# Kernel optimization log

Measured on AMD Instinct MI355X. Metric: run time of the kernel, lower is better.

Reference implementation:

```python
import jax, jax.numpy as jnp
import numpy as np

B, H, W, C = 32, 56, 56, 256
NH, WS, SHIFT = 8, 7, 3
S = WS * WS            # tokens per window = 49
CH = C // NH           # channels per head = 32
EPS = 1e-5


def layer_norm(x, w, b):
    mu = jnp.mean(x, axis=-1, keepdims=True)
    var = jnp.var(x, axis=-1, keepdims=True)
    return (x - mu) * jax.lax.rsqrt(var + EPS) * w + b


def spatial_mlp(x, weight, bias):
    # x: (B, H*W, C); weight: (NH*S, S, 1) grouped-conv1d weight; bias: (NH*S,)
    xr = x.reshape(B, H, W, C)
    if SHIFT > 0:
        P_l, P_r, P_t, P_b = WS - SHIFT, SHIFT, WS - SHIFT, SHIFT
        xr = jnp.pad(xr, ((0, 0), (P_t, P_b), (P_l, P_r), (0, 0)))
    Hp, Wp = xr.shape[1], xr.shape[2]
    # window partition -> (nW, S, NH, CH)
    win = xr.reshape(B, Hp // WS, WS, Wp // WS, WS, C)
    win = win.transpose(0, 1, 3, 2, 4, 5).reshape(-1, S, NH, CH)
    # grouped 1x1 conv == per-head token-mixing matrix (S x S)
    wgt = weight.reshape(NH, S, S)             # wgt[h, i, j]
    out = jnp.einsum('hij,njhd->nihd', wgt, win)
    out = out + bias.reshape(NH, S).T[None, :, :, None]
    # window reverse -> (B, Hp, Wp, C)
    out = out.reshape(B, Hp // WS, Wp // WS, WS, WS, C)
    out = out.transpose(0, 1, 3, 2, 4, 5).reshape(B, Hp, Wp, C)
    if SHIFT > 0:
        out = out[:, P_t:Hp - P_b, P_l:Wp - P_r, :]
    return out.reshape(B, H * W, C)


def mlp(x, fc1_w, fc1_b, fc2_w, fc2_b):
    h = jax.nn.gelu(x @ fc1_w + fc1_b, approximate=False)
    return h @ fc2_w + fc2_b


def setup_inputs() -> dict:
    key = jax.random.key(0)
    ks = jax.random.split(key, 5)
    sc = 0.02
    return {
        'x': jax.random.normal(ks[0], (B, H * W, C), jnp.float32),
        'norm1_w': jnp.ones((C,), jnp.float32),
        'norm1_b': jnp.zeros((C,), jnp.float32),
        'spatial_w': jax.random.normal(ks[1], (NH * S, S, 1), jnp.float32) * sc,
        'spatial_b': jax.random.normal(ks[2], (NH * S,), jnp.float32) * sc,
        'norm2_w': jnp.ones((C,), jnp.float32),
        'norm2_b': jnp.zeros((C,), jnp.float32),
        'fc1_w': jax.random.normal(ks[3], (C, 4 * C), jnp.float32) * sc,
        'fc1_b': jnp.zeros((4 * C,), jnp.float32),
        'fc2_w': jax.random.normal(ks[4], (4 * C, C), jnp.float32) * sc,
        'fc2_b': jnp.zeros((C,), jnp.float32),
    }


def reference(x, norm1_w, norm1_b, spatial_w, spatial_b, norm2_w, norm2_b,
              fc1_w, fc1_b, fc2_w, fc2_b):
    shortcut = x
    h = layer_norm(x, norm1_w, norm1_b)
    h = spatial_mlp(h, spatial_w, spatial_b)
    x = shortcut + h                      # drop_path = 0 (eval)
    x = x + mlp(layer_norm(x, norm2_w, norm2_b), fc1_w, fc1_b, fc2_w, fc2_b)
    return x
```

## Files before the change

### kernel.cpp

```cpp
#include <hip/hip_runtime.h>
#include <hip/hip_bf16.h>

#define NHEAD 8
#define IMG   3136
#define MTOT  100352

typedef __attribute__((ext_vector_type(2))) _Float16 f16x2;
typedef __attribute__((ext_vector_type(8))) _Float16 f16x8;
typedef __attribute__((ext_vector_type(4))) float    f32x4;
typedef __attribute__((ext_vector_type(16))) float   f32x16;
typedef __attribute__((ext_vector_type(8))) short    bf16x8;
typedef __attribute__((ext_vector_type(4))) short    s16x4;
typedef __attribute__((ext_vector_type(4))) int      i32x4;

#define SWZA(byteoff, r) ((byteoff) ^ (((r)&7)<<4) ^ ((((r)>>3)&1)<<7))

__device__ __forceinline__ short f2bf(float f){
  union { float fv; unsigned u; } a; a.fv = f;
  unsigned u = a.u;
  unsigned r = (u + 0x7fffu + ((u >> 16) & 1u)) >> 16;
  return (short)r;
}

__device__ __forceinline__ float dot2f16(f16x2 a, f16x2 b, float c){
#if __has_builtin(__builtin_amdgcn_fdot2)
  return __builtin_amdgcn_fdot2(a, b, c, false);
#else
  return c + (float)a[0]*(float)b[0] + (float)a[1]*(float)b[1];
#endif
}

__device__ __forceinline__ float gelu_f(float v){
  float u = v*(0.7978845608028654f + 0.0356774081f*(v*v));
  float e = __expf(2.f*u);
  float th = 1.f - 2.f/(e + 1.f);
  return 0.5f*v*(1.f + th);
}

__global__ void prep_k(const float* __restrict__ fc1w, const float* __restrict__ fc2w,
                       const float* __restrict__ spw,
                       short* __restrict__ w1p, short* __restrict__ w2p,
                       f16x2* __restrict__ wsp2)
{
  int bid = blockIdx.x, t = threadIdx.x;
  if (bid < 128) {
    int id = bid*256 + t;
    int l = id & 63, fk = id >> 6;
    int kk = fk & 15, f = fk >> 4;
    int n = f*32 + (l & 31);
    int kbase = kk*16 + (l >> 5)*8;
    bf16x8 o;
    #pragma unroll
    for (int e = 0; e < 8; ++e) o[e] = f2bf(fc1w[(size_t)(kbase+e)*1024 + n]);
    *(bf16x8*)(w1p + (size_t)id*8) = o;
  } else if (bid < 256) {
    int id = (bid-128)*256 + t;
    int l = id & 63, fk = id >> 6;
    int kk = fk & 63, f = fk >> 6;
    int n = f*32 + (l & 31);
    int kbase = kk*16 + (l >> 5)*8;
    bf16x8 o;
    #pragma unroll
    for (int e = 0; e < 8; ++e) o[e] = f2bf(fc2w[(size_t)(kbase+e)*256 + n]);
    *(bf16x8*)(w2p + (size_t)id*8) = o;
  } else {
    for (int idx = t; idx < 8*25*52; idx += 256) {
      int h = idx / 1300, rem = idx - h*1300;
      int jpp = rem / 52, i = rem - jpp*52;
      float lo = 0.f, hi = 0.f;
      if (i < 49) {
        int j0 = jpp*2;
        lo = spw[(size_t)(h*49 + i)*49 + j0];
        if (j0 + 1 < 49) hi = spw[(size_t)(h*49 + i)*49 + j0 + 1];
      }
      f16x2 v; v[0] = (_Float16)lo; v[1] = (_Float16)hi;
      wsp2[idx] = v;
    }
  }
}

__global__ __launch_bounds__(512,4) void win_k(
    const float* __restrict__ x, const float* __restrict__ n1w, const float* __restrict__ n1b,
    const float* __restrict__ spb, const f16x2* __restrict__ wsp2,
    float* __restrict__ x1)
{
  extern __shared__ char wsm[];
  char* lx = wsm;
  int t = threadIdx.x, lane = t & 63, wave = t >> 6;
  int bid = blockIdx.x;

  int wi_[2], wj_[2], b_[2];
  #pragma unroll
  for (int w = 0; w < 2; ++w) {
    int win = bid*2 + w;
    b_[w] = win/81; int rem = win - b_[w]*81;
    wi_[w] = rem/9; wj_[w] = rem - (rem/9)*9;
  }

  {
    i32x4 z4 = {0,0,0,0};
    i32x4* lx4 = (i32x4*)lx;
    for (int i = t; i < 3200; i += 512) lx4[i] = z4;
  }
  __syncthreads();

  f32x4 wv = *(const f32x4*)(n1w + lane*4);
  f32x4 bv = *(const f32x4*)(n1b + lane*4);
  #pragma unroll
  for (int w = 0; w < 2; ++w) {
    for (int i = wave; i < 49; i += 8) {
      int iy = i/7, ix = i - iy*7;
      int hh = wi_[w]*7 + iy - 4, ww = wj_[w]*7 + ix - 4;
      if (hh < 0 || hh >= 56 || ww < 0 || ww >= 56) continue;
      const float* row = x + ((size_t)(b_[w]*IMG + hh*56 + ww))*256;
      f32x4 v = *(const f32x4*)(row + lane*4);
      float s  = v[0]+v[1]+v[2]+v[3];
      float s2 = v[0]*v[0]+v[1]*v[1]+v[2]*v[2]+v[3]*v[3];
      #pragma unroll
      for (int m = 1; m < 64; m <<= 1) { s += __shfl_xor(s, m); s2 += __shfl_xor(s2, m); }
      float mu = s * (1.f/256.f);
      float rs = rsqrtf(s2*(1.f/256.f) - mu*mu + 1e-5f);
      char* base = lx + w*25600 + (i>>1)*1024 + (i&1)*2;
      #pragma unroll
      for (int q = 0; q < 4; ++q)
        *(_Float16*)(base + (lane*4+q)*4) = (_Float16)(((v[q]-mu)*rs)*wv[q] + bv[q]);
    }
  }
  __syncthreads();

  int h = __builtin_amdgcn_readfirstlane(wave);
  int d = lane & 31;
  int w = lane >> 5;
  int c = h*32 + d;
  const char* lxW = lx + w*25600 + c*4;
  const char* wgh = (const char*)wsp2 + h*5200;

  float acc[52];
  #pragma unroll
  for (int i = 0; i < 52; ++i) acc[i] = 0.f;

  for (int jpp = 0; jpp < 25; ++jpp) {
    f16x2 xa = *(const f16x2*)(lxW + jpp*1024);
    const char* wrow = wgh + jpp*208;
    #pragma unroll
    for (int ib = 0; ib < 13; ++ib) {
      f16x8 wq = *(const f16x8*)(wrow + ib*16);
      #pragma unroll
      for (int q = 0; q < 4; ++q) {
        f16x2 wp; wp[0] = wq[2*q]; wp[1] = wq[2*q+1];
        acc[ib*4+q] = dot2f16(wp, xa, acc[ib*4+q]);
      }
    }
  }

  int winW = bid*2 + w;
  int bW = winW/81, remW = winW - bW*81, wiW = remW/9, wjW = remW - (remW/9)*9;
  #pragma unroll
  for (int i = 0; i < 49; ++i) {
    int iy = i/7, ix = i - iy*7;
    float sb = spb[h*49 + i];
    int hh = wiW*7 + iy - 4, ww = wjW*7 + ix - 4;
    if (hh >= 0 && hh < 56 && ww >= 0 && ww < 56) {
      size_t off = ((size_t)(bW*IMG + hh*56 + ww))*256 + c;
      x1[off] = x[off] + acc[i] + sb;
    }
  }
}

__global__ __launch_bounds__(512,4) void mlp_k(
    const float* __restrict__ x1, float* __restrict__ out,
    const short* __restrict__ w1p, const short* __restrict__ w2p,
    const float* __restrict__ n2w, const float* __restrict__ n2b,
    const float* __restrict__ b1, const float* __restrict__ b2)
{
  extern __shared__ char sm[];
  char* a2  = sm;
  char* hcb = sm + 32768;

  int t = threadIdx.x, lane = t & 63, wave = t >> 6;
  int m0 = blockIdx.x * 64;

  {
    f32x4 nw = *(const f32x4*)(n2w + lane*4);
    f32x4 nb = *(const f32x4*)(n2b + lane*4);
    #pragma unroll
    for (int rq = 0; rq < 8; ++rq) {
      int rr = wave*8 + rq;
      f32x4 v = *(const f32x4*)(x1 + (size_t)(m0+rr)*256 + lane*4);
      float s  = v[0]+v[1]+v[2]+v[3];
      float s2 = v[0]*v[0]+v[1]*v[1]+v[2]*v[2]+v[3]*v[3];
      #pragma unroll
      for (int m = 1; m < 64; m <<= 1){ s += __shfl_xor(s,m); s2 += __shfl_xor(s2,m); }
      float mu = s*(1.f/256.f);
      float rs = rsqrtf(s2*(1.f/256.f) - mu*mu + 1e-5f);
      s16x4 pk;
      #pragma unroll
      for (int q = 0; q < 4; ++q) pk[q] = f2bf((v[q]-mu)*rs*nw[q] + nb[q]);
      *(s16x4*)(a2 + SWZA(lane*8, rr) + rr*512) = pk;
    }
  }
  __syncthreads();

  int lr = lane & 31, lk = lane >> 5;
  int wn = wave;

  f32x16 accO[2];
  #pragma unroll
  for (int i=0;i<2;++i)
    #pragma unroll
    for (int q=0;q<16;++q) accO[i][q] = 0.f;

  for (int ch = 0; ch < 4; ++ch) {
    f32x16 accH[2];
    #pragma unroll
    for (int i=0;i<2;++i)
      #pragma unroll
      for (int q=0;q<16;++q) accH[i][q] = 0.f;

    const short* w1f = w1p + ((size_t)((ch*8 + wn)*16)*64 + lane)*8;
    bf16x8 bq[4];
    #pragma unroll
    for (int k = 0; k < 4; ++k) bq[k] = *(const bf16x8*)(w1f + (size_t)k*512);
    __builtin_amdgcn_s_setprio(1);
    #pragma unroll
    for (int kk = 0; kk < 16; ++kk) {
      bf16x8 b = bq[kk & 3];
      if (kk < 12) bq[kk & 3] = *(const bf16x8*)(w1f + (size_t)(kk+4)*512);
      int kb = kk*32 + lk*16;
      bf16x8 a0 = *(const bf16x8*)(a2 + SWZA(kb, lr) + lr*512);
      bf16x8 a1 = *(const bf16x8*)(a2 + SWZA(kb, 32+lr) + (32+lr)*512);
      accH[0] = __builtin_amdgcn_mfma_f32_32x32x16_bf16(a0, b, accH[0], 0,0,0);
      accH[1] = __builtin_amdgcn_mfma_f32_32x32x16_bf16(a1, b, accH[1], 0,0,0);
    }
    __builtin_amdgcn_s_setprio(0);

    {
      float b1v = b1[ch*256 + wn*32 + lr];
      int colb = (wn*32 + lr)*2;
      #pragma unroll
      for (int ms = 0; ms < 2; ++ms) {
        #pragma unroll
        for (int r = 0; r < 16; ++r) {
          int rowl = ms*32 + (r&3) + 8*(r>>2) + 4*lk;
          float g = gelu_f(accH[ms][r] + b1v);
          *(short*)(hcb + SWZA(colb, rowl) + rowl*512) = f2bf(g);
        }
      }
    }
    __syncthreads();

    const short* w2f = w2p + ((size_t)(wn*64 + ch*16)*64 + lane)*8;
    #pragma unroll
    for (int k = 0; k < 4; ++k) bq[k] = *(const bf16x8*)(w2f + (size_t)k*512);
    __builtin_amdgcn_s_setprio(1);
    #pragma unroll
    for (int kk = 0; kk < 16; ++kk) {
      bf16x8 b = bq[kk & 3];
      if (kk < 12) bq[kk & 3] = *(const bf16x8*)(w2f + (size_t)(kk+4)*512);
      int kb = kk*32 + lk*16;
      bf16x8 a0 = *(const bf16x8*)(hcb + SWZA(kb, lr) + lr*512);
      bf16x8 a1 = *(const bf16x8*)(hcb + SWZA(kb, 32+lr) + (32+lr)*512);
      accO[0] = __builtin_amdgcn_mfma_f32_32x32x16_bf16(a0, b, accO[0], 0,0,0);
      accO[1] = __builtin_amdgcn_mfma_f32_32x32x16_bf16(a1, b, accO[1], 0,0,0);
    }
    __builtin_amdgcn_s_setprio(0);
    __syncthreads();
  }

  {
    int col = wn*32 + lr;
    float b2v = b2[col];
    #pragma unroll
    for (int ms = 0; ms < 2; ++ms) {
      #pragma unroll
      for (int r = 0; r < 16; ++r) {
        int row = ms*32 + (r&3) + 8*(r>>2) + 4*lk;
        size_t off = (size_t)(m0 + row)*256 + col;
        out[off] = x1[off] + accO[ms][r] + b2v;
      }
    }
  }
}

extern "C" void kernel_launch(void* const* d_in, const int* in_sizes, int n_in,
                              void* d_out, int out_size, void* d_ws, size_t ws_size,
                              hipStream_t stream) {
  const float* x    = (const float*)d_in[0];
  const float* n1w  = (const float*)d_in[1];
  const float* n1b  = (const float*)d_in[2];
  const float* spw  = (const float*)d_in[3];
  const float* spb  = (const float*)d_in[4];
  const float* n2w  = (const float*)d_in[5];
  const float* n2b  = (const float*)d_in[6];
  const float* fc1w = (const float*)d_in[7];
  const float* fc1b = (const float*)d_in[8];
  const float* fc2w = (const float*)d_in[9];
  const float* fc2b = (const float*)d_in[10];
  float* outp = (float*)d_out;

  char* ws = (char*)d_ws;
  short* w1p = (short*)ws;
  short* w2p = (short*)(ws + 524288);
  f16x2* wsp2 = (f16x2*)(ws + 1048576);

  prep_k<<<257, 256, 0, stream>>>(fc1w, fc2w, spw, w1p, w2p, wsp2);

  hipFuncSetAttribute(reinterpret_cast<const void*>(win_k),
                      hipFuncAttributeMaxDynamicSharedMemorySize, 51200);
  win_k<<<1296, 512, 51200, stream>>>(x, n1w, n1b, spb, wsp2, outp);

  hipFuncSetAttribute(reinterpret_cast<const void*>(mlp_k),
                      hipFuncAttributeMaxDynamicSharedMemorySize, 65536);
  mlp_k<<<MTOT/64, 512, 65536, stream>>>(outp, outp, w1p, w2p, n2w, n2b, fc1b, fc2b);
}
```

Baseline: 334.1 us.

## Use bf16 MFMA for window token-mixing instead of fdot2 scalar loops

The per-head 49x49 token-mixing in win_k now runs as bf16 32x32x16 MFMA tiles, padded to 64x64, instead of per-lane fdot2 accumulation over 52 registers. Weights are pre-packed into the MFMA A-operand layout in prep_k. LayerNorm stats are computed first, then normalized activations are written transposed and swizzled into LDS as bf16. This cuts VALU work and register pressure, at the cost of more LDS (66KB per block, which may reduce occupancy), lower precision (bf16 instead of fp16), and uncoalesced per-channel reads of x during the transpose.

```diff
diff --git a/kernel.cpp b/kernel.cpp
--- a/kernel.cpp
+++ b/kernel.cpp
@@ -22,14 +22,6 @@
   return (short)r;
 }
 
-__device__ __forceinline__ float dot2f16(f16x2 a, f16x2 b, float c){
-#if __has_builtin(__builtin_amdgcn_fdot2)
-  return __builtin_amdgcn_fdot2(a, b, c, false);
-#else
-  return c + (float)a[0]*(float)b[0] + (float)a[1]*(float)b[1];
-#endif
-}
-
 __device__ __forceinline__ float gelu_f(float v){
   float u = v*(0.7978845608028654f + 0.0356774081f*(v*v));
   float e = __expf(2.f*u);
@@ -40,7 +32,7 @@
 __global__ void prep_k(const float* __restrict__ fc1w, const float* __restrict__ fc2w,
                        const float* __restrict__ spw,
                        short* __restrict__ w1p, short* __restrict__ w2p,
-                       f16x2* __restrict__ wsp2)
+                       short* __restrict__ wspA)
 {
   int bid = blockIdx.x, t = threadIdx.x;
   if (bid < 128) {
@@ -64,55 +56,47 @@
     for (int e = 0; e < 8; ++e) o[e] = f2bf(fc2w[(size_t)(kbase+e)*256 + n]);
     *(bf16x8*)(w2p + (size_t)id*8) = o;
   } else {
-    for (int idx = t; idx < 8*25*52; idx += 256) {
-      int h = idx / 1300, rem = idx - h*1300;
-      int jpp = rem / 52, i = rem - jpp*52;
-      float lo = 0.f, hi = 0.f;
-      if (i < 49) {
-        int j0 = jpp*2;
-        lo = spw[(size_t)(h*49 + i)*49 + j0];
-        if (j0 + 1 < 49) hi = spw[(size_t)(h*49 + i)*49 + j0 + 1];
-      }
-      f16x2 v; v[0] = (_Float16)lo; v[1] = (_Float16)hi;
-      wsp2[idx] = v;
+    #pragma unroll
+    for (int k = 0; k < 16; ++k) {
+      int idx = t + k*256;
+      int lane = idx & 63;
+      int kt = (idx >> 6) & 3;
+      int mt = (idx >> 8) & 1;
+      int h  = idx >> 9;
+      int i  = mt*32 + (lane & 31);
+      int jb = kt*16 + (lane >> 5)*8;
+      bf16x8 o;
+      #pragma unroll
+      for (int e = 0; e < 8; ++e) {
+        int j = jb + e;
+        float v = (i < 49 && j < 49) ? spw[(size_t)(h*49 + i)*49 + j] : 0.f;
+        o[e] = f2bf(v);
+      }
+      *(bf16x8*)(wspA + (size_t)idx*8) = o;
     }
   }
 }
 
 __global__ __launch_bounds__(512,4) void win_k(
     const float* __restrict__ x, const float* __restrict__ n1w, const float* __restrict__ n1b,
-    const float* __restrict__ spb, const f16x2* __restrict__ wsp2,
+    const float* __restrict__ spb, const short* __restrict__ wspA,
     float* __restrict__ x1)
 {
   extern __shared__ char wsm[];
-  char* lx = wsm;
+  char*  lxT  = wsm;
+  float* murs = (float*)(wsm + 65536);
   int t = threadIdx.x, lane = t & 63, wave = t >> 6;
   int bid = blockIdx.x;
 
-  int wi_[2], wj_[2], b_[2];
   #pragma unroll
   for (int w = 0; w < 2; ++w) {
     int win = bid*2 + w;
-    b_[w] = win/81; int rem = win - b_[w]*81;
-    wi_[w] = rem/9; wj_[w] = rem - (rem/9)*9;
-  }
-
-  {
-    i32x4 z4 = {0,0,0,0};
-    i32x4* lx4 = (i32x4*)lx;
-    for (int i = t; i < 3200; i += 512) lx4[i] = z4;
-  }
-  __syncthreads();
-
-  f32x4 wv = *(const f32x4*)(n1w + lane*4);
-  f32x4 bv = *(const f32x4*)(n1b + lane*4);
-  #pragma unroll
-  for (int w = 0; w < 2; ++w) {
+    int b = win/81, rem = win - b*81, wi = rem/9, wj = rem - (rem/9)*9;
     for (int i = wave; i < 49; i += 8) {
       int iy = i/7, ix = i - iy*7;
-      int hh = wi_[w]*7 + iy - 4, ww = wj_[w]*7 + ix - 4;
+      int hh = wi*7 + iy - 4, ww = wj*7 + ix - 4;
       if (hh < 0 || hh >= 56 || ww < 0 || ww >= 56) continue;
-      const float* row = x + ((size_t)(b_[w]*IMG + hh*56 + ww))*256;
+      const float* row = x + ((size_t)(b*IMG + hh*56 + ww))*256;
       f32x4 v = *(const f32x4*)(row + lane*4);
       float s  = v[0]+v[1]+v[2]+v[3];
       float s2 = v[0]*v[0]+v[1]*v[1]+v[2]*v[2]+v[3]*v[3];
@@ -120,49 +104,80 @@
       for (int m = 1; m < 64; m <<= 1) { s += __shfl_xor(s, m); s2 += __shfl_xor(s2, m); }
       float mu = s * (1.f/256.f);
       float rs = rsqrtf(s2*(1.f/256.f) - mu*mu + 1e-5f);
-      char* base = lx + w*25600 + (i>>1)*1024 + (i&1)*2;
-      #pragma unroll
-      for (int q = 0; q < 4; ++q)
-        *(_Float16*)(base + (lane*4+q)*4) = (_Float16)(((v[q]-mu)*rs)*wv[q] + bv[q]);
+      if (lane == 0) { murs[(w*56+i)*2] = mu; murs[(w*56+i)*2+1] = rs; }
     }
   }
   __syncthreads();
 
-  int h = __builtin_amdgcn_readfirstlane(wave);
-  int d = lane & 31;
-  int w = lane >> 5;
+  {
+    int w = t >> 8, c = t & 255;
+    int win = bid*2 + w;
+    int b = win/81, rem = win - b*81, wi = rem/9, wj = rem - (rem/9)*9;
+    float nwc = n1w[c], nbc = n1b[c];
+    char* rowb = lxT + c*256;
+    #pragma unroll
+    for (int cj = 0; cj < 7; ++cj) {
+      bf16x8 pk;
+      #pragma unroll
+      for (int e = 0; e < 8; ++e) {
+        int p = cj*8 + e;
+        short val = 0;
+        if (p < 49) {
+          int iy = p/7, ix = p - iy*7;
+          int hh = wi*7 + iy - 4, ww = wj*7 + ix - 4;
+          if (hh >= 0 && hh < 56 && ww >= 0 && ww < 56) {
+            float mu = murs[(w*56+p)*2], rs = murs[(w*56+p)*2+1];
+            float xv = x[((size_t)(b*IMG + hh*56 + ww))*256 + c];
+            val = f2bf((xv - mu)*rs*nwc + nbc);
+          }
+        }
+        pk[e] = val;
+      }
+      *(bf16x8*)(rowb + SWZA(w*128 + cj*16, c)) = pk;
+    }
+    bf16x8 z = {0,0,0,0,0,0,0,0};
+    *(bf16x8*)(rowb + SWZA(w*128 + 112, c)) = z;
+  }
+  __syncthreads();
+
+  int h = wave, d = lane & 31, lk = lane >> 5;
+  const short* wA = wspA + h*4096;
   int c = h*32 + d;
-  const char* lxW = lx + w*25600 + c*4;
-  const char* wgh = (const char*)wsp2 + h*5200;
-
-  float acc[52];
-  #pragma unroll
-  for (int i = 0; i < 52; ++i) acc[i] = 0.f;
-
-  for (int jpp = 0; jpp < 25; ++jpp) {
-    f16x2 xa = *(const f16x2*)(lxW + jpp*1024);
-    const char* wrow = wgh + jpp*208;
-    #pragma unroll
-    for (int ib = 0; ib < 13; ++ib) {
-      f16x8 wq = *(const f16x8*)(wrow + ib*16);
-      #pragma unroll
-      for (int q = 0; q < 4; ++q) {
-        f16x2 wp; wp[0] = wq[2*q]; wp[1] = wq[2*q+1];
-        acc[ib*4+q] = dot2f16(wp, xa, acc[ib*4+q]);
-      }
-    }
-  }
-
-  int winW = bid*2 + w;
-  int bW = winW/81, remW = winW - bW*81, wiW = remW/9, wjW = remW - (remW/9)*9;
-  #pragma unroll
-  for (int i = 0; i < 49; ++i) {
-    int iy = i/7, ix = i - iy*7;
-    float sb = spb[h*49 + i];
-    int hh = wiW*7 + iy - 4, ww = wjW*7 + ix - 4;
-    if (hh >= 0 && hh < 56 && ww >= 0 && ww < 56) {
-      size_t off = ((size_t)(bW*IMG + hh*56 + ww))*256 + c;
-      x1[off] = x[off] + acc[i] + sb;
+  f32x16 a00, a01, a10, a11;
+  #pragma unroll
+  for (int q = 0; q < 16; ++q) { a00[q]=0.f; a01[q]=0.f; a10[q]=0.f; a11[q]=0.f; }
+  #pragma unroll
+  for (int kt = 0; kt < 4; ++kt) {
+    bf16x8 A0 = *(const bf16x8*)(wA + (kt*64 + lane)*8);
+    bf16x8 A1 = *(const bf16x8*)(wA + ((4+kt)*64 + lane)*8);
+    int bo = kt*32 + lk*16;
+    bf16x8 B0 = *(const bf16x8*)(lxT + c*256 + SWZA(bo, c));
+    bf16x8 B1 = *(const bf16x8*)(lxT + c*256 + SWZA(128 + bo, c));
+    a00 = __builtin_amdgcn_mfma_f32_32x32x16_bf16(A0, B0, a00, 0,0,0);
+    a10 = __builtin_amdgcn_mfma_f32_32x32x16_bf16(A1, B0, a10, 0,0,0);
+    a01 = __builtin_amdgcn_mfma_f32_32x32x16_bf16(A0, B1, a01, 0,0,0);
+    a11 = __builtin_amdgcn_mfma_f32_32x32x16_bf16(A1, B1, a11, 0,0,0);
+  }
+
+  #pragma unroll
+  for (int w = 0; w < 2; ++w) {
+    int win = bid*2 + w;
+    int b = win/81, rem = win - b*81, wi = rem/9, wj = rem - (rem/9)*9;
+    #pragma unroll
+    for (int mt = 0; mt < 2; ++mt) {
+      #pragma unroll
+      for (int r = 0; r < 16; ++r) {
+        int i = mt*32 + (r&3) + 8*(r>>2) + 4*lk;
+        if (i < 49) {
+          int iy = i/7, ix = i - iy*7;
+          int hh = wi*7 + iy - 4, ww = wj*7 + ix - 4;
+          if (hh >= 0 && hh < 56 && ww >= 0 && ww < 56) {
+            size_t off = ((size_t)(b*IMG + hh*56 + ww))*256 + c;
+            float av = mt==0 ? (w==0 ? a00[r] : a01[r]) : (w==0 ? a10[r] : a11[r]);
+            x1[off] = x[off] + av + spb[h*49 + i];
+          }
+        }
+      }
     }
   }
 }
@@ -299,15 +314,15 @@
   float* outp = (float*)d_out;
 
   char* ws = (char*)d_ws;
-  short* w1p = (short*)ws;
-  short* w2p = (short*)(ws + 524288);
-  f16x2* wsp2 = (f16x2*)(ws + 1048576);
-
-  prep_k<<<257, 256, 0, stream>>>(fc1w, fc2w, spw, w1p, w2p, wsp2);
+  short* w1p  = (short*)ws;
+  short* w2p  = (short*)(ws + 524288);
+  short* wspA = (short*)(ws + 1048576);
+
+  prep_k<<<257, 256, 0, stream>>>(fc1w, fc2w, spw, w1p, w2p, wspA);
 
   hipFuncSetAttribute(reinterpret_cast<const void*>(win_k),
-                      hipFuncAttributeMaxDynamicSharedMemorySize, 51200);
-  win_k<<<1296, 512, 51200, stream>>>(x, n1w, n1b, spb, wsp2, outp);
+                      hipFuncAttributeMaxDynamicSharedMemorySize, 66432);
+  win_k<<<1296, 512, 66432, stream>>>(x, n1w, n1b, spb, wspA, outp);
 
   hipFuncSetAttribute(reinterpret_cast<const void*>(mlp_k),
                       hipFuncAttributeMaxDynamicSharedMemorySize, 65536);
```

Result: faster. 318.7 us (-4.6%).
